# Kernel optimization log

Measured on AMD Instinct MI355X. Metric: run time of the kernel, lower is better.

The kernel has to match this reference:

```python
import jax, jax.numpy as jnp
import numpy as np

D_MODEL = 1024
N_HEADS = 16
HEAD_DIM = D_MODEL // N_HEADS
BATCH = 1
SEQLEN = 4096


def setup_inputs() -> dict:
    key = jax.random.key(0)
    k1, k2, k3 = jax.random.split(key, 3)
    x = jax.random.normal(k1, (BATCH, SEQLEN, D_MODEL), dtype=jnp.float32)
    # match typical Dense init scale so softmax isn't saturated
    Wqkv = jax.random.normal(k2, (D_MODEL, 3 * D_MODEL), dtype=jnp.float32) / np.sqrt(D_MODEL)
    Wout = jax.random.normal(k3, (D_MODEL, D_MODEL), dtype=jnp.float32) / np.sqrt(D_MODEL)
    return {"x": x, "Wqkv": Wqkv, "Wout": Wout}


def reference(x, Wqkv, Wout):
    b, l, d = x.shape
    qkv = x @ Wqkv  # [b, l, 3d]
    q, k, v = jnp.split(qkv, 3, axis=-1)
    # [b, l, d] -> [b, h, l, hd]
    def to_heads(t):
        return t.reshape(b, l, N_HEADS, HEAD_DIM).transpose(0, 2, 1, 3)
    q, k, v = to_heads(q), to_heads(k), to_heads(v)
    scale = 1.0 / np.sqrt(HEAD_DIM)
    attn = jnp.einsum('bhld,bhsd->bhls', q, k) * scale  # [b,h,l,l]
    causal_mask = jnp.tril(jnp.ones((l, l), dtype=bool))
    attn = jnp.where(causal_mask, attn, -jnp.inf)
    attn = jax.nn.softmax(attn, axis=-1)
    out = jnp.einsum('bhls,bhsd->bhld', attn, v)  # [b,h,l,hd]
    out = out.transpose(0, 2, 1, 3).reshape(b, l, d)
    return out @ Wout
```

## Files before the change

kernel.cpp:

```cpp
#include <hip/hip_runtime.h>

#define SEQ 4096
#define DM 1024
#define NH 16
#define HD 64

typedef __attribute__((ext_vector_type(8))) short short8;
typedef __attribute__((ext_vector_type(4))) short short4v;
typedef __attribute__((ext_vector_type(2))) short short2v;
typedef __attribute__((ext_vector_type(4))) float float4v;
typedef __attribute__((ext_vector_type(4))) int int4v;

__device__ __forceinline__ short f2bf(float f) {
    union { float f; unsigned u; } v; v.f = f;
    unsigned u = v.u;
    return (short)((u + 0x7fffu + ((u >> 16) & 1u)) >> 16);
}
__device__ __forceinline__ int pk2bf(float a, float b) {
    union { float f; unsigned u; } x, y; x.f = a; y.f = b;
    return (int)__builtin_amdgcn_perm(y.u + 0x8000u, x.u + 0x8000u, 0x07060302u);
}

__device__ __forceinline__ void gload_lds16(const void* g, void* l) {
    __builtin_amdgcn_global_load_lds(
        (const __attribute__((address_space(1))) void*)g,
        (__attribute__((address_space(3))) void*)l, 16, 0, 0);
}

__global__ void cast_x(const float* __restrict__ in, short* __restrict__ out, int n4) {
    int i = blockIdx.x * blockDim.x + threadIdx.x;
    if (i < n4) {
        float4v x = ((const float4v*)in)[i];
        short4v o;
        o[0] = f2bf(x[0]); o[1] = f2bf(x[1]); o[2] = f2bf(x[2]); o[3] = f2bf(x[3]);
        ((short4v*)out)[i] = o;
    }
}

__global__ void transpose_cast(const float* __restrict__ in, short* __restrict__ out,
                               int H, int W, int scaled_rows, float scale) {
    __shared__ float tile[32][33];
    int bx = blockIdx.x * 32, by = blockIdx.y * 32;
    int tx = threadIdx.x, ty = threadIdx.y;
#pragma unroll
    for (int i = 0; i < 32; i += 8)
        tile[ty + i][tx] = in[(by + ty + i) * W + bx + tx];
    __syncthreads();
#pragma unroll
    for (int i = 0; i < 32; i += 8) {
        int orow = bx + ty + i;
        float sc = (orow < scaled_rows) ? scale : 1.0f;
        out[orow * H + by + tx] = f2bf(tile[tx][ty + i] * sc);
    }
}

__global__ void transpose_v(const short* __restrict__ qkv, short* __restrict__ vt) {
    __shared__ short tile[64][66];
    int h = blockIdx.z;
    int l0 = blockIdx.x * 64;
    int tx = threadIdx.x, ty = threadIdx.y;
#pragma unroll
    for (int i = 0; i < 8; i++) {
        int r = ty + i * 8;
        short2v v = *(const short2v*)&qkv[(l0 + r) * (3 * DM) + 2 * DM + h * HD + 2 * tx];
        tile[r][2 * tx] = v[0];
        tile[r][2 * tx + 1] = v[1];
    }
    __syncthreads();
#pragma unroll
    for (int i = 0; i < 8; i++) {
        int d = ty + i * 8;
        short2v v;
        v[0] = tile[2 * tx][d];
        v[1] = tile[2 * tx + 1][d];
        int s = l0 + 2 * tx;
        int soff = (s & ~31) | ((s & 12) << 1) | ((s & 16) >> 2) | (s & 3);
        *(short2v*)&vt[(h * HD + d) * SEQ + soff] = v;
    }
}

template <typename OutT>
__global__ __launch_bounds__(256) void gemm_bt(const short* __restrict__ A,
                                               const short* __restrict__ BT,
                                               OutT* __restrict__ C,
                                               int M, int N, int K) {
    __shared__ short As[128 * 32];
    __shared__ short Bs[128 * 32];
    int tid  = threadIdx.x;
    int m0   = blockIdx.y * 128;
    int n0   = blockIdx.x * 128;
    int w    = tid >> 6, lane = tid & 63;
    int wm   = w >> 1,  wn   = w & 1;
    int quad = lane >> 4, l15 = lane & 15;
    int srow = lane >> 2;
    int scol = (lane & 3) * 8;

    float4v acc[4][4];
#pragma unroll
    for (int mi = 0; mi < 4; mi++)
#pragma unroll
        for (int ni = 0; ni < 4; ni++)
            acc[mi][ni] = {0.f, 0.f, 0.f, 0.f};

    for (int k0 = 0; k0 < K; k0 += 32) {
        __syncthreads();
#pragma unroll
        for (int t = 0; t < 2; t++) {
            int chunk = w * 2 + t;
            int r = chunk * 16 + srow;
            gload_lds16(&A[(m0 + r) * K + k0 + scol], &As[chunk * 16 * 32]);
            gload_lds16(&BT[(n0 + r) * K + k0 + scol], &Bs[chunk * 16 * 32]);
        }
        __syncthreads();
        short8 a[4], b[4];
#pragma unroll
        for (int mi = 0; mi < 4; mi++)
            a[mi] = *(const short8*)&As[(wm * 64 + mi * 16 + l15) * 32 + quad * 8];
#pragma unroll
        for (int ni = 0; ni < 4; ni++)
            b[ni] = *(const short8*)&Bs[(wn * 64 + ni * 16 + l15) * 32 + quad * 8];
#pragma unroll
        for (int mi = 0; mi < 4; mi++)
#pragma unroll
            for (int ni = 0; ni < 4; ni++)
                acc[mi][ni] = __builtin_amdgcn_mfma_f32_16x16x32_bf16(a[mi], b[ni], acc[mi][ni], 0, 0, 0);
    }

#pragma unroll
    for (int mi = 0; mi < 4; mi++)
#pragma unroll
        for (int ni = 0; ni < 4; ni++)
#pragma unroll
            for (int r = 0; r < 4; r++) {
                int row = m0 + wm * 64 + mi * 16 + quad * 4 + r;
                int col = n0 + wn * 64 + ni * 16 + l15;
                float v = acc[mi][ni][r];
                if constexpr (sizeof(OutT) == 2) C[row * N + col] = (OutT)f2bf(v);
                else                             C[row * N + col] = (OutT)v;
            }
}

__global__ __launch_bounds__(256) void gemm_bt64(const short* __restrict__ A,
                                                 const short* __restrict__ BT,
                                                 float* __restrict__ C,
                                                 int M, int N, int K) {
    __shared__ short As[64 * 32];
    __shared__ short Bs[128 * 32];
    int tid  = threadIdx.x;
    int m0   = blockIdx.y * 64;
    int n0   = blockIdx.x * 128;
    int w    = tid >> 6, lane = tid & 63;
    int wm   = w >> 1,  wn   = w & 1;
    int quad = lane >> 4, l15 = lane & 15;
    int srow = lane >> 2;
    int scol = (lane & 3) * 8;

    float4v acc[2][4];
#pragma unroll
    for (int mi = 0; mi < 2; mi++)
#pragma unroll
        for (int ni = 0; ni < 4; ni++)
            acc[mi][ni] = {0.f, 0.f, 0.f, 0.f};

    for (int k0 = 0; k0 < K; k0 += 32) {
        __syncthreads();
        {
            int r = w * 16 + srow;
            gload_lds16(&A[(m0 + r) * K + k0 + scol], &As[w * 16 * 32]);
        }
#pragma unroll
        for (int t = 0; t < 2; t++) {
            int chunk = w * 2 + t;
            int r = chunk * 16 + srow;
            gload_lds16(&BT[(n0 + r) * K + k0 + scol], &Bs[chunk * 16 * 32]);
        }
        __syncthreads();
        short8 a[2], b[4];
#pragma unroll
        for (int mi = 0; mi < 2; mi++)
            a[mi] = *(const short8*)&As[(wm * 32 + mi * 16 + l15) * 32 + quad * 8];
#pragma unroll
        for (int ni = 0; ni < 4; ni++)
            b[ni] = *(const short8*)&Bs[(wn * 64 + ni * 16 + l15) * 32 + quad * 8];
#pragma unroll
        for (int mi = 0; mi < 2; mi++)
#pragma unroll
            for (int ni = 0; ni < 4; ni++)
                acc[mi][ni] = __builtin_amdgcn_mfma_f32_16x16x32_bf16(a[mi], b[ni], acc[mi][ni], 0, 0, 0);
    }

#pragma unroll
    for (int mi = 0; mi < 2; mi++)
#pragma unroll
        for (int ni = 0; ni < 4; ni++)
#pragma unroll
            for (int r = 0; r < 4; r++) {
                int row = m0 + wm * 32 + mi * 16 + quad * 4 + r;
                int col = n0 + wn * 64 + ni * 16 + l15;
                C[row * N + col] = acc[mi][ni][r];
            }
}

__global__ __launch_bounds__(256) void attn_kernel(const short* __restrict__ qkv,
                                                   const short* __restrict__ vtp,
                                                   float* __restrict__ Of0,
                                                   float* __restrict__ Of1,
                                                   float* __restrict__ Lf0,
                                                   float* __restrict__ Lf1) {
    __shared__ short Ks[64 * 72];
    __shared__ short Vs[64 * 72];
    int gid = blockIdx.x;
    int rr = gid & 7, qq = gid >> 3;
    int hb = qq >> 5, b = qq & 31;
    int h = rr + 8 * hb;
    int tid = threadIdx.x;
    int w = tid >> 6, lane = tid & 63;
    int quad = lane >> 4, l15 = lane & 15;
    int r8 = lane >> 3, c8 = lane & 7;
    int srow = w * 16 + r8;

    const short* Kg = qkv + DM + h * HD;
    const short* Vg = vtp + (h * HD) * SEQ;

#pragma unroll 1
    for (int job = 0; job < 2; job++) {
        int t   = job ? (31 - b) : b;
        int st0 = job ? (t + 1) : 0;
        int stN = job ? (2 * t + 2) : (t + 1);
        float* __restrict__ Of = job ? Of1 : Of0;
        float* __restrict__ Lf = job ? Lf1 : Lf0;
        int q0 = t * 128;
        int qw = q0 + w * 32;

        short8 aq[2][2];
#pragma unroll
        for (int mi = 0; mi < 2; mi++)
#pragma unroll
            for (int kk = 0; kk < 2; kk++)
                aq[mi][kk] = *(const short8*)&qkv[(qw + mi * 16 + l15) * (3 * DM) + h * HD + kk * 32 + quad * 8];

        float lp[2] = {0.f, 0.f};
        float4v o[2][4];
#pragma unroll
        for (int mi = 0; mi < 2; mi++)
#pragma unroll
            for (int dt = 0; dt < 4; dt++)
                o[mi][dt] = {0.f, 0.f, 0.f, 0.f};

        short8 kg[2], vg[2];
        int sb = st0 * 64;
#pragma unroll
        for (int i = 0; i < 2; i++) {
            kg[i] = *(const short8*)&Kg[(sb + srow + 8 * i) * (3 * DM) + c8 * 8];
            vg[i] = *(const short8*)&Vg[(srow + 8 * i) * SEQ + sb + c8 * 8];
        }

        for (int tt = st0; tt < stN; tt++) {
            int s0 = tt * 64;
            int sn = (tt + 1 < stN) ? s0 + 64 : s0;

            __syncthreads();
#pragma unroll
            for (int i = 0; i < 2; i++) {
                *(short8*)&Ks[(srow + 8 * i) * 72 + c8 * 8] = kg[i];
                *(short8*)&Vs[(srow + 8 * i) * 72 + c8 * 8] = vg[i];
            }
#pragma unroll
            for (int i = 0; i < 2; i++) {
                kg[i] = *(const short8*)&Kg[(sn + srow + 8 * i) * (3 * DM) + c8 * 8];
                vg[i] = *(const short8*)&Vg[(srow + 8 * i) * SEQ + sn + c8 * 8];
            }
            __syncthreads();

            short8 kc[8], vc[8];
#pragma unroll
            for (int ni = 0; ni < 4; ni++)
#pragma unroll
                for (int kk = 0; kk < 2; kk++)
                    kc[ni * 2 + kk] = *(const short8*)&Ks[(ni * 16 + l15) * 72 + kk * 32 + quad * 8];
#pragma unroll
            for (int dt = 0; dt < 4; dt++)
#pragma unroll
                for (int pr = 0; pr < 2; pr++)
                    vc[dt * 2 + pr] = *(const short8*)&Vs[(dt * 16 + l15) * 72 + pr * 32 + quad * 8];

            float4v s[2][4];
#pragma unroll
            for (int mi = 0; mi < 2; mi++)
#pragma unroll
                for (int ni = 0; ni < 4; ni++) {
                    float4v a = {0.f, 0.f, 0.f, 0.f};
#pragma unroll
                    for (int kk = 0; kk < 2; kk++)
                        a = __builtin_amdgcn_mfma_f32_16x16x32_bf16(kc[ni * 2 + kk], aq[mi][kk], a, 0, 0, 0);
                    s[mi][ni] = a;
                }

            bool diag = (s0 + 63 > qw);
            short8 pa[2][2];
#pragma unroll
            for (int mi = 0; mi < 2; mi++) {
                int qrow = qw + mi * 16 + l15;
#pragma unroll
                for (int ni = 0; ni < 4; ni++) {
#pragma unroll
                    for (int r = 0; r < 4; r++) {
                        float p = __builtin_amdgcn_exp2f(s[mi][ni][r]);
                        if (diag) {
                            int scol = s0 + ni * 16 + quad * 4 + r;
                            p = (scol <= qrow) ? p : 0.f;
                        }
                        lp[mi] += p;
                        s[mi][ni][r] = p;
                    }
                }
#pragma unroll
                for (int pr = 0; pr < 2; pr++) {
                    int4v wpk;
                    wpk[0] = pk2bf(s[mi][2 * pr][0], s[mi][2 * pr][1]);
                    wpk[1] = pk2bf(s[mi][2 * pr][2], s[mi][2 * pr][3]);
                    wpk[2] = pk2bf(s[mi][2 * pr + 1][0], s[mi][2 * pr + 1][1]);
                    wpk[3] = pk2bf(s[mi][2 * pr + 1][2], s[mi][2 * pr + 1][3]);
                    pa[mi][pr] = *(short8*)&wpk;
                }
            }
#pragma unroll
            for (int mi = 0; mi < 2; mi++)
#pragma unroll
                for (int dt = 0; dt < 4; dt++)
#pragma unroll
                    for (int pr = 0; pr < 2; pr++)
                        o[mi][dt] = __builtin_amdgcn_mfma_f32_16x16x32_bf16(pa[mi][pr], vc[dt * 2 + pr], o[mi][dt], 0, 0, 0);
        }

#pragma unroll
        for (int mi = 0; mi < 2; mi++) {
            lp[mi] += __shfl_xor(lp[mi], 16, 64);
            lp[mi] += __shfl_xor(lp[mi], 32, 64);
        }
#pragma unroll
        for (int mi = 0; mi < 2; mi++)
#pragma unroll
            for (int r = 0; r < 4; r++) {
                int row = qw + mi * 16 + quad * 4 + r;
#pragma unroll
                for (int dt = 0; dt < 4; dt++)
                    Of[row * DM + h * HD + dt * 16 + l15] = o[mi][dt][r];
            }
        if (quad == 0) {
#pragma unroll
            for (int mi = 0; mi < 2; mi++)
                Lf[h * SEQ + qw + mi * 16 + l15] = lp[mi];
        }
    }
}

__global__ void attn_finalize(const float* __restrict__ Of0, const float* __restrict__ Of1,
                              const float* __restrict__ Lf0, const float* __restrict__ Lf1,
                              short* __restrict__ ao) {
    int i = blockIdx.x * blockDim.x + threadIdx.x;
    int q  = i >> 8;
    int c4 = i & 255;
    int h  = c4 >> 4;
    float l = Lf0[h * SEQ + q] + Lf1[h * SEQ + q];
    float inv = 1.0f / l;
    float4v a = ((const float4v*)Of0)[i];
    float4v bv = ((const float4v*)Of1)[i];
    short4v o;
    o[0] = f2bf((a[0] + bv[0]) * inv);
    o[1] = f2bf((a[1] + bv[1]) * inv);
    o[2] = f2bf((a[2] + bv[2]) * inv);
    o[3] = f2bf((a[3] + bv[3]) * inv);
    ((short4v*)ao)[i] = o;
}

extern "C" void kernel_launch(void* const* d_in, const int* in_sizes, int n_in,
                              void* d_out, int out_size, void* d_ws, size_t ws_size,
                              hipStream_t stream) {
    const float* x    = (const float*)d_in[0];
    const float* Wqkv = (const float*)d_in[1];
    const float* Wout = (const float*)d_in[2];
    float* out = (float*)d_out;

    char* ws = (char*)d_ws;
    short* xb    = (short*)(ws);
    short* wqkvT = (short*)(ws + 8388608);
    float* Of0   = (float*)(ws);
    short* qkv   = (short*)(ws + 16777216);
    short* vt    = (short*)(ws + 16777216 + 25165824);
    short* ao    = (short*)(ws + 16777216 + 25165824 + 8388608);
    float* Of1   = (float*)(ws + 58720256);
    float* Lf0   = (float*)(ws + 75497472);
    float* Lf1   = (float*)(ws + 75759616);
    short* woutT = (short*)(ws + 76021760);

    const float SC = 0.18033688011112042f;

    cast_x<<<4096, 256, 0, stream>>>(x, xb, (SEQ * DM) / 4);
    transpose_cast<<<dim3(3 * DM / 32, DM / 32), dim3(32, 8), 0, stream>>>(Wqkv, wqkvT, DM, 3 * DM, DM, SC);
    transpose_cast<<<dim3(DM / 32, DM / 32), dim3(32, 8), 0, stream>>>(Wout, woutT, DM, DM, 0, 1.0f);

    gemm_bt<short><<<dim3(3 * DM / 128, SEQ / 128), 256, 0, stream>>>(xb, wqkvT, qkv, SEQ, 3 * DM, DM);

    transpose_v<<<dim3(SEQ / 64, 1, NH), dim3(32, 8), 0, stream>>>(qkv, vt);

    attn_kernel<<<512, 256, 0, stream>>>(qkv, vt, Of0, Of1, Lf0, Lf1);
    attn_finalize<<<(SEQ * DM / 4) / 256, 256, 0, stream>>>(Of0, Of1, Lf0, Lf1, ao);

    gemm_bt64<<<dim3(DM / 128, SEQ / 64), 256, 0, stream>>>(ao, woutT, out, SEQ, DM, DM);
}
```

Before: 214.5 us.

## Split attention work into three balanced KV partitions and use MFMA row sums

Attention work is redistributed from 512 blocks covering paired causal query tiles to 768 blocks. Each block processes a fixed 22-tile slice of the combined KV range for a query-tile pair, which gives more even load across CUs. Softmax row sums now come from an MFMA against a ones vector instead of scalar adds and shuffles. Bf16 packing uses the hardware v_cvt_pk_bf16_f32 instruction, and the double __syncthreads is replaced by explicit waitcnt/barrier pairs. The change adds a third partial output buffer (aliased onto d_out) and more complex finalize logic. It also changes rounding behavior slightly.

```diff
diff --git a/kernel.cpp b/kernel.cpp
--- a/kernel.cpp
+++ b/kernel.cpp
@@ -16,9 +16,10 @@
     unsigned u = v.u;
     return (short)((u + 0x7fffu + ((u >> 16) & 1u)) >> 16);
 }
-__device__ __forceinline__ int pk2bf(float a, float b) {
-    union { float f; unsigned u; } x, y; x.f = a; y.f = b;
-    return (int)__builtin_amdgcn_perm(y.u + 0x8000u, x.u + 0x8000u, 0x07060302u);
+__device__ __forceinline__ int cvtpk(float lo, float hi) {
+    int r;
+    asm("v_cvt_pk_bf16_f32 %0, %1, %2" : "=v"(r) : "v"(lo), "v"(hi));
+    return r;
 }
 
 __device__ __forceinline__ void gload_lds16(const void* g, void* l) {
@@ -205,14 +206,23 @@
                                                    const short* __restrict__ vtp,
                                                    float* __restrict__ Of0,
                                                    float* __restrict__ Of1,
+                                                   float* __restrict__ Of2,
                                                    float* __restrict__ Lf0,
-                                                   float* __restrict__ Lf1) {
+                                                   float* __restrict__ Lf1,
+                                                   float* __restrict__ Lf2) {
     __shared__ short Ks[64 * 72];
     __shared__ short Vs[64 * 72];
     int gid = blockIdx.x;
     int rr = gid & 7, qq = gid >> 3;
-    int hb = qq >> 5, b = qq & 31;
+    int hb = qq / 48;
+    int rem = qq - hb * 48;
     int h = rr + 8 * hb;
+    int b = rem & 15;
+    int j = rem >> 4;
+    float* __restrict__ Of = (j == 0) ? Of0 : (j == 1) ? Of1 : Of2;
+    float* __restrict__ Lf = (j == 0) ? Lf0 : (j == 1) ? Lf1 : Lf2;
+    int B0 = 2 * b + 2;
+
     int tid = threadIdx.x;
     int w = tid >> 6, lane = tid & 63;
     int quad = lane >> 4, l15 = lane & 15;
@@ -222,13 +232,25 @@
     const short* Kg = qkv + DM + h * HD;
     const short* Vg = vtp + (h * HD) * SEQ;
 
+    short8 onesv;
+#pragma unroll
+    for (int i = 0; i < 8; i++) onesv[i] = (short)0x3F80;
+
 #pragma unroll 1
-    for (int job = 0; job < 2; job++) {
-        int t   = job ? (31 - b) : b;
-        int st0 = job ? (t + 1) : 0;
-        int stN = job ? (2 * t + 2) : (t + 1);
-        float* __restrict__ Of = job ? Of1 : Of0;
-        float* __restrict__ Lf = job ? Lf1 : Lf0;
+    for (int sg = 0; sg < 2; sg++) {
+        int t, st0, stN;
+        if (sg == 0) {
+            t = b;
+            st0 = 22 * j;
+            stN = (22 * j + 22 < B0) ? 22 * j + 22 : B0;
+        } else {
+            t = 31 - b;
+            int a0 = 22 * j - B0;
+            st0 = (a0 > 0) ? a0 : 0;
+            stN = 22 * j + 22 - B0;
+        }
+        if (st0 >= stN) continue;
+
         int q0 = t * 128;
         int qw = q0 + w * 32;
 
@@ -239,13 +261,15 @@
             for (int kk = 0; kk < 2; kk++)
                 aq[mi][kk] = *(const short8*)&qkv[(qw + mi * 16 + l15) * (3 * DM) + h * HD + kk * 32 + quad * 8];
 
-        float lp[2] = {0.f, 0.f};
+        float4v lacc[2];
         float4v o[2][4];
 #pragma unroll
-        for (int mi = 0; mi < 2; mi++)
+        for (int mi = 0; mi < 2; mi++) {
+            lacc[mi] = {0.f, 0.f, 0.f, 0.f};
 #pragma unroll
             for (int dt = 0; dt < 4; dt++)
                 o[mi][dt] = {0.f, 0.f, 0.f, 0.f};
+        }
 
         short8 kg[2], vg[2];
         int sb = st0 * 64;
@@ -259,18 +283,20 @@
             int s0 = tt * 64;
             int sn = (tt + 1 < stN) ? s0 + 64 : s0;
 
-            __syncthreads();
 #pragma unroll
             for (int i = 0; i < 2; i++) {
                 *(short8*)&Ks[(srow + 8 * i) * 72 + c8 * 8] = kg[i];
                 *(short8*)&Vs[(srow + 8 * i) * 72 + c8 * 8] = vg[i];
             }
+            asm volatile("s_waitcnt lgkmcnt(0)" ::: "memory");
+            __builtin_amdgcn_s_barrier();
+            __builtin_amdgcn_sched_barrier(0);
+
 #pragma unroll
             for (int i = 0; i < 2; i++) {
                 kg[i] = *(const short8*)&Kg[(sn + srow + 8 * i) * (3 * DM) + c8 * 8];
                 vg[i] = *(const short8*)&Vg[(srow + 8 * i) * SEQ + sn + c8 * 8];
             }
-            __syncthreads();
 
             short8 kc[8], vc[8];
 #pragma unroll
@@ -310,34 +336,37 @@
                             int scol = s0 + ni * 16 + quad * 4 + r;
                             p = (scol <= qrow) ? p : 0.f;
                         }
-                        lp[mi] += p;
                         s[mi][ni][r] = p;
                     }
                 }
 #pragma unroll
                 for (int pr = 0; pr < 2; pr++) {
                     int4v wpk;
-                    wpk[0] = pk2bf(s[mi][2 * pr][0], s[mi][2 * pr][1]);
-                    wpk[1] = pk2bf(s[mi][2 * pr][2], s[mi][2 * pr][3]);
-                    wpk[2] = pk2bf(s[mi][2 * pr + 1][0], s[mi][2 * pr + 1][1]);
-                    wpk[3] = pk2bf(s[mi][2 * pr + 1][2], s[mi][2 * pr + 1][3]);
+                    wpk[0] = cvtpk(s[mi][2 * pr][0], s[mi][2 * pr][1]);
+                    wpk[1] = cvtpk(s[mi][2 * pr][2], s[mi][2 * pr][3]);
+                    wpk[2] = cvtpk(s[mi][2 * pr + 1][0], s[mi][2 * pr + 1][1]);
+                    wpk[3] = cvtpk(s[mi][2 * pr + 1][2], s[mi][2 * pr + 1][3]);
                     pa[mi][pr] = *(short8*)&wpk;
                 }
             }
 #pragma unroll
             for (int mi = 0; mi < 2; mi++)
 #pragma unroll
+                for (int pr = 0; pr < 2; pr++)
+                    lacc[mi] = __builtin_amdgcn_mfma_f32_16x16x32_bf16(pa[mi][pr], onesv, lacc[mi], 0, 0, 0);
+#pragma unroll
+            for (int mi = 0; mi < 2; mi++)
+#pragma unroll
                 for (int dt = 0; dt < 4; dt++)
 #pragma unroll
                     for (int pr = 0; pr < 2; pr++)
                         o[mi][dt] = __builtin_amdgcn_mfma_f32_16x16x32_bf16(pa[mi][pr], vc[dt * 2 + pr], o[mi][dt], 0, 0, 0);
-        }
-
-#pragma unroll
-        for (int mi = 0; mi < 2; mi++) {
-            lp[mi] += __shfl_xor(lp[mi], 16, 64);
-            lp[mi] += __shfl_xor(lp[mi], 32, 64);
-        }
+
+            asm volatile("s_waitcnt lgkmcnt(0)" ::: "memory");
+            __builtin_amdgcn_s_barrier();
+            __builtin_amdgcn_sched_barrier(0);
+        }
+
 #pragma unroll
         for (int mi = 0; mi < 2; mi++)
 #pragma unroll
@@ -347,30 +376,55 @@
                 for (int dt = 0; dt < 4; dt++)
                     Of[row * DM + h * HD + dt * 16 + l15] = o[mi][dt][r];
             }
-        if (quad == 0) {
+        if (l15 == 0) {
 #pragma unroll
             for (int mi = 0; mi < 2; mi++)
-                Lf[h * SEQ + qw + mi * 16 + l15] = lp[mi];
+#pragma unroll
+                for (int r = 0; r < 4; r++)
+                    Lf[h * SEQ + qw + mi * 16 + quad * 4 + r] = lacc[mi][r];
         }
     }
 }
 
 __global__ void attn_finalize(const float* __restrict__ Of0, const float* __restrict__ Of1,
+                              const float* __restrict__ Of2,
                               const float* __restrict__ Lf0, const float* __restrict__ Lf1,
+                              const float* __restrict__ Lf2,
                               short* __restrict__ ao) {
     int i = blockIdx.x * blockDim.x + threadIdx.x;
     int q  = i >> 8;
     int c4 = i & 255;
     int h  = c4 >> 4;
-    float l = Lf0[h * SEQ + q] + Lf1[h * SEQ + q];
+    int t  = q >> 7;
+    bool lowq = (t < 16);
+    int b = lowq ? t : 31 - t;
+    bool use0 = lowq || (b <= 9);
+    bool use1 = (!lowq) || (b >= 11);
+    bool use2 = !lowq;
+
+    float l = 0.f;
+    float4v acc = {0.f, 0.f, 0.f, 0.f};
+    if (use0) {
+        l += Lf0[h * SEQ + q];
+        float4v a = ((const float4v*)Of0)[i];
+        acc[0] += a[0]; acc[1] += a[1]; acc[2] += a[2]; acc[3] += a[3];
+    }
+    if (use1) {
+        l += Lf1[h * SEQ + q];
+        float4v a = ((const float4v*)Of1)[i];
+        acc[0] += a[0]; acc[1] += a[1]; acc[2] += a[2]; acc[3] += a[3];
+    }
+    if (use2) {
+        l += Lf2[h * SEQ + q];
+        float4v a = ((const float4v*)Of2)[i];
+        acc[0] += a[0]; acc[1] += a[1]; acc[2] += a[2]; acc[3] += a[3];
+    }
     float inv = 1.0f / l;
-    float4v a = ((const float4v*)Of0)[i];
-    float4v bv = ((const float4v*)Of1)[i];
     short4v o;
-    o[0] = f2bf((a[0] + bv[0]) * inv);
-    o[1] = f2bf((a[1] + bv[1]) * inv);
-    o[2] = f2bf((a[2] + bv[2]) * inv);
-    o[3] = f2bf((a[3] + bv[3]) * inv);
+    o[0] = f2bf(acc[0] * inv);
+    o[1] = f2bf(acc[1] * inv);
+    o[2] = f2bf(acc[2] * inv);
+    o[3] = f2bf(acc[3] * inv);
     ((short4v*)ao)[i] = o;
 }
 
@@ -386,13 +440,15 @@
     short* xb    = (short*)(ws);
     short* wqkvT = (short*)(ws + 8388608);
     float* Of0   = (float*)(ws);
+    float* Of1   = (float*)(d_out);
     short* qkv   = (short*)(ws + 16777216);
-    short* vt    = (short*)(ws + 16777216 + 25165824);
-    short* ao    = (short*)(ws + 16777216 + 25165824 + 8388608);
-    float* Of1   = (float*)(ws + 58720256);
+    short* vt    = (short*)(ws + 41943040);
+    short* ao    = (short*)(ws + 50331648);
+    float* Of2   = (float*)(ws + 58720256);
     float* Lf0   = (float*)(ws + 75497472);
     float* Lf1   = (float*)(ws + 75759616);
-    short* woutT = (short*)(ws + 76021760);
+    float* Lf2   = (float*)(ws + 76021760);
+    short* woutT = (short*)(ws + 76283904);
 
     const float SC = 0.18033688011112042f;
 
@@ -404,8 +460,8 @@
 
     transpose_v<<<dim3(SEQ / 64, 1, NH), dim3(32, 8), 0, stream>>>(qkv, vt);
 
-    attn_kernel<<<512, 256, 0, stream>>>(qkv, vt, Of0, Of1, Lf0, Lf1);
-    attn_finalize<<<(SEQ * DM / 4) / 256, 256, 0, stream>>>(Of0, Of1, Lf0, Lf1, ao);
+    attn_kernel<<<768, 256, 0, stream>>>(qkv, vt, Of0, Of1, Of2, Lf0, Lf1, Lf2);
+    attn_finalize<<<(SEQ * DM / 4) / 256, 256, 0, stream>>>(Of0, Of1, Of2, Lf0, Lf1, Lf2, ao);
 
     gemm_bt64<<<dim3(DM / 128, SEQ / 64), 256, 0, stream>>>(ao, woutT, out, SEQ, DM, DM);
 }
```

Result: faster. 209.9 us (-2.1%).
